# Kernel tuning notes

Hardware: AMD Instinct MI355X
Metric: run time of the kernel (lower is better)

Reference implementation:

```python
import jax, jax.numpy as jnp
import numpy as np

B, S, E, H = 8, 1024, 768, 12
D = E // H  # per-head dim


def setup_inputs() -> dict:
    key = jax.random.key(0)
    ks = jax.random.split(key, 9)
    glorot = lambda k: jax.random.normal(k, (E, E), jnp.float32) * np.sqrt(2.0 / (E + E))
    return {
        "inputs": jax.random.normal(ks[0], (B, S, E), jnp.float32),
        "Wq": glorot(ks[1]), "bq": jnp.zeros((E,), jnp.float32),
        "Wk": glorot(ks[2]), "bk": jnp.zeros((E,), jnp.float32),
        "Wv": glorot(ks[3]), "bv": jnp.zeros((E,), jnp.float32),
        "Wo": glorot(ks[4]), "bo": jnp.zeros((E,), jnp.float32),
    }


def reference(inputs, Wq, bq, Wk, bk, Wv, bv, Wo, bo):
    b, s, e = inputs.shape
    # QKV projections then split heads: [B,S,E] -> [B,H,S,D]
    def heads(x):
        return x.reshape(b, s, H, D).transpose(0, 2, 1, 3)
    q = heads(inputs @ Wq + bq)
    k = heads(inputs @ Wk + bk)
    v = heads(inputs @ Wv + bv)
    scale = 1.0 / jnp.sqrt(jnp.asarray(D, inputs.dtype))
    scores = jnp.einsum("bhqd,bhkd->bhqk", q, k) * scale
    weights = jax.nn.softmax(scores, axis=-1)  # attn_drop rate 0 -> identity
    attn = jnp.einsum("bhqk,bhkd->bhqd", weights, v)
    concat = attn.transpose(0, 2, 1, 3).reshape(b, s, e)
    out = concat @ Wo + bo  # proj_drop rate 0 -> identity
    return out
```

## Files before the change

kernel.cpp:

```cpp
#include <hip/hip_runtime.h>
#include <math.h>

#define BB 8
#define SS 1024
#define EE 768
#define HH 12
#define DD 64
#define MM (BB*SS)

typedef __attribute__((ext_vector_type(8))) short short8;
typedef __attribute__((ext_vector_type(4))) short short4v;
typedef __attribute__((ext_vector_type(4))) float f32x4;

static __device__ __forceinline__ short f2bf(float x) {
    unsigned u = __float_as_uint(x);
    u += 0x7fffu + ((u >> 16) & 1u);
    return (short)(u >> 16);
}
static __device__ __forceinline__ short f2bf_fast(float x) {
    return (short)((__float_as_uint(x) + 0x8000u) >> 16);
}

static __device__ __forceinline__ void gload_lds16(const void* g, void* l) {
    __builtin_amdgcn_global_load_lds((__attribute__((address_space(1))) void*)g,
                                     (__attribute__((address_space(3))) void*)l,
                                     16, 0, 0);
}

__global__ __launch_bounds__(256)
void cast_x(const float* __restrict__ src, short* __restrict__ dst) {
    const long i = ((long)blockIdx.x * 256 + threadIdx.x) * 4;
    float4 v = *(const float4*)&src[i];
    short4v o;
    o.x = f2bf(v.x); o.y = f2bf(v.y); o.z = f2bf(v.z); o.w = f2bf(v.w);
    *(short4v*)&dst[i] = o;
}

__global__ __launch_bounds__(256)
void wcast_t(const float* __restrict__ W0, const float* __restrict__ W1,
             const float* __restrict__ W2, const float* __restrict__ W3,
             short* __restrict__ Wt) {
    __shared__ short T[64][72];
    const int z = blockIdx.z;
    const float* sp = (z == 0) ? W0 : (z == 1) ? W1 : (z == 2) ? W2 : W3;
    short* dp = Wt + (long)z * EE * EE;
    const int i0 = blockIdx.y * 64;
    const int j0 = blockIdx.x * 64;
    const int tid = threadIdx.x;
#pragma unroll
    for (int rep = 0; rep < 4; ++rep) {
        const int r = (tid >> 4) + rep * 16;
        const int c = (tid & 15) * 4;
        float4 v = *(const float4*)&sp[(long)(i0 + r) * EE + j0 + c];
        T[c + 0][r] = f2bf(v.x);
        T[c + 1][r] = f2bf(v.y);
        T[c + 2][r] = f2bf(v.z);
        T[c + 3][r] = f2bf(v.w);
    }
    __syncthreads();
#pragma unroll
    for (int rep = 0; rep < 4; ++rep) {
        const int rr = (tid >> 4) + rep * 16;
        const int cc = (tid & 15) * 4;
        short4v o;
        o.x = T[rr][cc + 0]; o.y = T[rr][cc + 1];
        o.z = T[rr][cc + 2]; o.w = T[rr][cc + 3];
        *(short4v*)&dp[(long)(j0 + rr) * EE + i0 + cc] = o;
    }
}

#define GEMM_CORE(Abase, Bbase, row0, col0)                                     \
    f32x4 acc[4][4];                                                            \
    _Pragma("unroll") for (int i = 0; i < 4; ++i)                               \
        _Pragma("unroll") for (int j = 0; j < 4; ++j)                           \
            acc[i][j] = (f32x4){0.f, 0.f, 0.f, 0.f};                            \
    const int rm = (w & 1) * 64, cn = (w >> 1) * 64;                            \
    for (int k0 = 0; k0 < EE; k0 += 64) {                                       \
        __syncthreads();                                                        \
        _Pragma("unroll") for (int i = 0; i < 4; ++i) {                         \
            const int chunk = w * 256 + i * 64 + lane;                          \
            const int r = chunk >> 3;                                           \
            const int cs = (((chunk & 7) ^ (r & 7)) << 3);                      \
            short* ldsA = Al + (w * 256 + i * 64) * 8;                          \
            short* ldsB = Bl + (w * 256 + i * 64) * 8;                          \
            gload_lds16(&Abase[(long)(row0 + r) * EE + k0 + cs], ldsA);         \
            gload_lds16(&Bbase[(long)(col0 + r) * EE + k0 + cs], ldsB);         \
        }                                                                       \
        __syncthreads();                                                        \
        _Pragma("unroll") for (int ks = 0; ks < 2; ++ks) {                      \
            short8 af[4], bf[4];                                                \
            _Pragma("unroll") for (int t = 0; t < 4; ++t)                       \
                af[t] = *(const short8*)&Al[(rm + t * 16 + m) * 64 +            \
                                            (((ks * 4 + quad) ^ (m & 7)) << 3)]; \
            _Pragma("unroll") for (int t = 0; t < 4; ++t)                       \
                bf[t] = *(const short8*)&Bl[(cn + t * 16 + m) * 64 +            \
                                            (((ks * 4 + quad) ^ (m & 7)) << 3)]; \
            _Pragma("unroll") for (int mt = 0; mt < 4; ++mt)                    \
                _Pragma("unroll") for (int nt = 0; nt < 4; ++nt)                \
                    acc[mt][nt] = __builtin_amdgcn_mfma_f32_16x16x32_bf16(      \
                        af[mt], bf[nt], acc[mt][nt], 0, 0, 0);                  \
        }                                                                       \
    }

#define TSTRIDE 134

#define QSCALE 0.1803368801111204f

__global__ __launch_bounds__(256)
void gemm_qkv(const short* __restrict__ Xb, const short* __restrict__ Wt,
              const float* __restrict__ bq, const float* __restrict__ bk,
              const float* __restrict__ bv,
              short* __restrict__ Qb, short* __restrict__ Kb,
              short* __restrict__ Vb) {
    __shared__ short SMEM[128 * TSTRIDE];
    short* const Al = SMEM;
    short* const Bl = SMEM + 128 * 64;
    const int tid = threadIdx.x, w = tid >> 6, lane = tid & 63;
    const int m = lane & 15, quad = lane >> 4;
    const int wsel = blockIdx.x / 6;
    const int colt = blockIdx.x % 6;
    const int row0 = blockIdx.y * 128;
    const int col0 = colt * 128;
    const short* Wsel = Wt + (long)wsel * EE * EE;
    const float* bias = (wsel == 0) ? bq : (wsel == 1) ? bk : bv;

    GEMM_CORE(Xb, Wsel, row0, col0)

    __syncthreads();
    const int b = row0 >> 10, s0 = row0 & 1023;

    if (wsel < 2) {
        const float scale = (wsel == 0) ? QSCALE : 1.0f;
        short* QK = (wsel == 0) ? Qb : Kb;
#pragma unroll
        for (int nt = 0; nt < 4; ++nt) {
            const float bvv = bias[col0 + cn + nt * 16 + m];
#pragma unroll
            for (int mt = 0; mt < 4; ++mt)
#pragma unroll
                for (int r = 0; r < 4; ++r)
                    SMEM[(rm + mt * 16 + quad * 4 + r) * TSTRIDE + cn + nt * 16 + m] =
                        f2bf((acc[mt][nt][r] + bvv) * scale);
        }
        __syncthreads();
#pragma unroll
        for (int rep = 0; rep < 8; ++rep) {
            const int chunk = tid + rep * 256;
            const int row = chunk >> 4;
            const int cc = (chunk & 15) * 8;
            const int colg = col0 + cc;
            const int h = colg >> 6, d = colg & 63;
            short8 v = *(const short8*)&SMEM[row * TSTRIDE + cc];
            *(short8*)&QK[((long)(b * HH + h) * SS + s0 + row) * DD + d] = v;
        }
    } else {
#pragma unroll
        for (int nt = 0; nt < 4; ++nt) {
            const float bvv = bias[col0 + cn + nt * 16 + m];
#pragma unroll
            for (int mt = 0; mt < 4; ++mt) {
                const int rowb = rm + mt * 16 + quad * 4;
                short4v o;
                o.x = f2bf(acc[mt][nt][0] + bvv);
                o.y = f2bf(acc[mt][nt][1] + bvv);
                o.z = f2bf(acc[mt][nt][2] + bvv);
                o.w = f2bf(acc[mt][nt][3] + bvv);
                *(short4v*)&SMEM[(cn + nt * 16 + m) * TSTRIDE + rowb] = o;
            }
        }
        __syncthreads();
#pragma unroll
        for (int rep = 0; rep < 8; ++rep) {
            const int chunk = tid + rep * 256;
            const int col = chunk >> 4;
            const int sc8 = (chunk & 15) * 8;
            const int colg = col0 + col;
            const int h = colg >> 6, d = colg & 63;
            short8 v = *(const short8*)&SMEM[col * TSTRIDE + sc8];
            *(short8*)&Vb[((long)(b * HH + h) * DD + d) * SS + s0 + sc8] = v;
        }
    }
}

__global__ __launch_bounds__(256)
void gemm_proj(const short* __restrict__ Cb, const short* __restrict__ WoT,
               const float* __restrict__ bo, float* __restrict__ out) {
    __shared__ short Al[128 * 64];
    __shared__ short Bl[128 * 64];
    const int tid = threadIdx.x, w = tid >> 6, lane = tid & 63;
    const int m = lane & 15, quad = lane >> 4;
    const int row0 = blockIdx.y * 128;
    const int col0 = blockIdx.x * 128;

    GEMM_CORE(Cb, WoT, row0, col0)

#pragma unroll
    for (int nt = 0; nt < 4; ++nt) {
        const int colg = col0 + cn + nt * 16 + m;
        const float bvv = bo[colg];
#pragma unroll
        for (int mt = 0; mt < 4; ++mt)
#pragma unroll
            for (int r = 0; r < 4; ++r) {
                const int srow = row0 + rm + mt * 16 + quad * 4 + r;
                out[(long)srow * EE + colg] = acc[mt][nt][r] + bvv;
            }
    }
}

__global__ __launch_bounds__(256)
void attn_mfma(const short* __restrict__ Q,
               const short* __restrict__ K,
               const short* __restrict__ Vt,
               short* __restrict__ out) {
    __shared__ short Kl[64 * 72];
    __shared__ short Vl[64 * 72];
    __shared__ short Pl[4 * 32 * 72];

    const int tid  = threadIdx.x;
    const int w    = tid >> 6;
    const int l    = tid & 63;
    const int m    = l & 15;
    const int quad = l >> 4;
    const int h = blockIdx.y, b = blockIdx.z;
    const int q0 = blockIdx.x * 128;
    const long bh = (long)(b * HH + h);

    const short* Qg = Q  + bh * SS * DD;
    const short* Kg = K  + bh * SS * DD;
    const short* Vg = Vt + bh * DD * SS;

    short8 aq[2][2];
#pragma unroll
    for (int g = 0; g < 2; ++g) {
        const int row = q0 + w * 32 + g * 16 + m;
        aq[g][0] = *(const short8*)(Qg + (long)row * DD + quad * 8);
        aq[g][1] = *(const short8*)(Qg + (long)row * DD + 32 + quad * 8);
    }

    short8 ones;
#pragma unroll
    for (int i = 0; i < 8; ++i) ones[i] = (short)0x3F80;

    f32x4 O[2][4], lacc[2];
#pragma unroll
    for (int g = 0; g < 2; ++g) {
        lacc[g] = (f32x4){0.f, 0.f, 0.f, 0.f};
#pragma unroll
        for (int dt = 0; dt < 4; ++dt) O[g][dt] = (f32x4){0.f, 0.f, 0.f, 0.f};
    }

    for (int kt = 0; kt < 16; ++kt) {
        const int k0 = kt * 64;
        __syncthreads();
#pragma unroll
        for (int rep = 0; rep < 2; ++rep) {
            const int seg = tid + rep * 256;
            const int r = seg >> 3, s = seg & 7;
            *(short8*)(Kl + r * 72 + s * 8) =
                *(const short8*)(Kg + (long)(k0 + r) * DD + s * 8);
            *(short8*)(Vl + r * 72 + s * 8) =
                *(const short8*)(Vg + (long)r * SS + k0 + s * 8);
        }
        __syncthreads();

        f32x4 sc[2][4];
#pragma unroll
        for (int nt = 0; nt < 4; ++nt) {
            const short* kb = Kl + (nt * 16 + m) * 72 + quad * 8;
            short8 b0 = *(const short8*)kb;
            short8 b1 = *(const short8*)(kb + 32);
#pragma unroll
            for (int g = 0; g < 2; ++g) {
                f32x4 a = (f32x4){0.f, 0.f, 0.f, 0.f};
                a = __builtin_amdgcn_mfma_f32_16x16x32_bf16(aq[g][0], b0, a, 0, 0, 0);
                a = __builtin_amdgcn_mfma_f32_16x16x32_bf16(aq[g][1], b1, a, 0, 0, 0);
                sc[g][nt] = a;
            }
        }

#pragma unroll
        for (int g = 0; g < 2; ++g)
#pragma unroll
            for (int nt = 0; nt < 4; ++nt)
#pragma unroll
                for (int r = 0; r < 4; ++r)
                    sc[g][nt][r] = __builtin_amdgcn_exp2f(sc[g][nt][r]);

        short* Pw = Pl + w * 32 * 72;
#pragma unroll
        for (int g = 0; g < 2; ++g)
#pragma unroll
            for (int nt = 0; nt < 4; ++nt)
#pragma unroll
                for (int r = 0; r < 4; ++r)
                    Pw[(g * 16 + quad * 4 + r) * 72 + nt * 16 + m] =
                        f2bf_fast(sc[g][nt][r]);

        short8 ap[2][2];
#pragma unroll
        for (int g = 0; g < 2; ++g) {
            ap[g][0] = *(const short8*)(Pw + (g * 16 + m) * 72 + quad * 8);
            ap[g][1] = *(const short8*)(Pw + (g * 16 + m) * 72 + 32 + quad * 8);
        }

#pragma unroll
        for (int g = 0; g < 2; ++g) {
            lacc[g] = __builtin_amdgcn_mfma_f32_16x16x32_bf16(ap[g][0], ones, lacc[g], 0, 0, 0);
            lacc[g] = __builtin_amdgcn_mfma_f32_16x16x32_bf16(ap[g][1], ones, lacc[g], 0, 0, 0);
        }
#pragma unroll
        for (int dt = 0; dt < 4; ++dt) {
            const short* vb = Vl + (dt * 16 + m) * 72 + quad * 8;
            short8 b0 = *(const short8*)vb;
            short8 b1 = *(const short8*)(vb + 32);
#pragma unroll
            for (int g = 0; g < 2; ++g) {
                O[g][dt] = __builtin_amdgcn_mfma_f32_16x16x32_bf16(ap[g][0], b0, O[g][dt], 0, 0, 0);
                O[g][dt] = __builtin_amdgcn_mfma_f32_16x16x32_bf16(ap[g][1], b1, O[g][dt], 0, 0, 0);
            }
        }
    }

#pragma unroll
    for (int g = 0; g < 2; ++g)
#pragma unroll
        for (int r = 0; r < 4; ++r) {
            const float inv = 1.0f / lacc[g][r];
            const int qo = q0 + w * 32 + g * 16 + quad * 4 + r;
            short* orow = out + ((long)(b * SS + qo)) * EE + h * DD;
#pragma unroll
            for (int dt = 0; dt < 4; ++dt)
                orow[dt * 16 + m] = f2bf(O[g][dt][r] * inv);
        }
}

extern "C" void kernel_launch(void* const* d_in, const int* in_sizes, int n_in,
                              void* d_out, int out_size, void* d_ws, size_t ws_size,
                              hipStream_t stream) {
    const float* X  = (const float*)d_in[0];
    const float* Wq = (const float*)d_in[1];
    const float* bq = (const float*)d_in[2];
    const float* Wk = (const float*)d_in[3];
    const float* bk = (const float*)d_in[4];
    const float* Wv = (const float*)d_in[5];
    const float* bv = (const float*)d_in[6];
    const float* Wo = (const float*)d_in[7];
    const float* bo = (const float*)d_in[8];

    const long SEG = (long)BB * HH * SS * DD;
    const long WSEG = (long)EE * EE;
    short* Xb = (short*)d_ws;
    short* Wt = Xb + SEG;
    short* Qb = Wt + 4 * WSEG;
    short* Kb = Qb + SEG;
    short* Vb = Kb + SEG;
    short* Cb = Vb + SEG;

    cast_x<<<dim3(MM * EE / 4 / 256), 256, 0, stream>>>(X, Xb);
    wcast_t<<<dim3(12, 12, 4), 256, 0, stream>>>(Wq, Wk, Wv, Wo, Wt);

    gemm_qkv<<<dim3(18, 64), 256, 0, stream>>>(Xb, Wt, bq, bk, bv, Qb, Kb, Vb);

    attn_mfma<<<dim3(SS / 128, HH, BB), 256, 0, stream>>>(Qb, Kb, Vb, Cb);

    gemm_proj<<<dim3(6, 64), 256, 0, stream>>>(Cb, Wt + 3 * WSEG, bo,
                                               (float*)d_out);
}
```

Before: 216.1 us.

## Merge cast kernels, swap MFMA operands for vectorized epilogues, pad LDS strides

Folds the X cast and the weight transpose-cast into one prep launch, which saves a kernel launch. The Q/K and output-projection GEMMs swap the MFMA operands so each lane holds 4 consecutive columns. That lets the bias be read as a float4 and results be written as short4 or float4 instead of scalar stores. LDS strides for the QKV transpose buffer and the attention P buffer change to reduce bank conflicts. The risk is that the altered layouts introduce new conflicts and that the merged prep kernel branches on block index.

```diff
diff --git a/kernel.cpp b/kernel.cpp
--- a/kernel.cpp
+++ b/kernel.cpp
@@ -27,26 +27,30 @@
                                      16, 0, 0);
 }
 
+#define XB (MM * EE / 4 / 256)
+
 __global__ __launch_bounds__(256)
-void cast_x(const float* __restrict__ src, short* __restrict__ dst) {
-    const long i = ((long)blockIdx.x * 256 + threadIdx.x) * 4;
-    float4 v = *(const float4*)&src[i];
-    short4v o;
-    o.x = f2bf(v.x); o.y = f2bf(v.y); o.z = f2bf(v.z); o.w = f2bf(v.w);
-    *(short4v*)&dst[i] = o;
-}
-
-__global__ __launch_bounds__(256)
-void wcast_t(const float* __restrict__ W0, const float* __restrict__ W1,
-             const float* __restrict__ W2, const float* __restrict__ W3,
-             short* __restrict__ Wt) {
+void prep(const float* __restrict__ X,
+          const float* __restrict__ W0, const float* __restrict__ W1,
+          const float* __restrict__ W2, const float* __restrict__ W3,
+          short* __restrict__ Xb, short* __restrict__ Wt) {
     __shared__ short T[64][72];
-    const int z = blockIdx.z;
+    const int tid = threadIdx.x;
+    if ((int)blockIdx.x < XB) {
+        const long i = ((long)blockIdx.x * 256 + tid) * 4;
+        float4 v = *(const float4*)&X[i];
+        short4v o;
+        o.x = f2bf(v.x); o.y = f2bf(v.y); o.z = f2bf(v.z); o.w = f2bf(v.w);
+        *(short4v*)&Xb[i] = o;
+        return;
+    }
+    const int idx = blockIdx.x - XB;
+    const int z = idx / 144;
+    const int rem = idx % 144;
+    const int i0 = (rem / 12) * 64;
+    const int j0 = (rem % 12) * 64;
     const float* sp = (z == 0) ? W0 : (z == 1) ? W1 : (z == 2) ? W2 : W3;
     short* dp = Wt + (long)z * EE * EE;
-    const int i0 = blockIdx.y * 64;
-    const int j0 = blockIdx.x * 64;
-    const int tid = threadIdx.x;
 #pragma unroll
     for (int rep = 0; rep < 4; ++rep) {
         const int r = (tid >> 4) + rep * 16;
@@ -69,7 +73,7 @@
     }
 }
 
-#define GEMM_CORE(Abase, Bbase, row0, col0)                                     \
+#define GEMM_CORE(Abase, Bbase, row0, col0, SWAP)                               \
     f32x4 acc[4][4];                                                            \
     _Pragma("unroll") for (int i = 0; i < 4; ++i)                               \
         _Pragma("unroll") for (int j = 0; j < 4; ++j)                           \
@@ -97,12 +101,15 @@
                                             (((ks * 4 + quad) ^ (m & 7)) << 3)]; \
             _Pragma("unroll") for (int mt = 0; mt < 4; ++mt)                    \
                 _Pragma("unroll") for (int nt = 0; nt < 4; ++nt)                \
-                    acc[mt][nt] = __builtin_amdgcn_mfma_f32_16x16x32_bf16(      \
-                        af[mt], bf[nt], acc[mt][nt], 0, 0, 0);                  \
+                    acc[mt][nt] = (SWAP)                                        \
+                        ? __builtin_amdgcn_mfma_f32_16x16x32_bf16(              \
+                              bf[nt], af[mt], acc[mt][nt], 0, 0, 0)             \
+                        : __builtin_amdgcn_mfma_f32_16x16x32_bf16(              \
+                              af[mt], bf[nt], acc[mt][nt], 0, 0, 0);            \
         }                                                                       \
     }
 
-#define TSTRIDE 134
+#define TS 140
 
 #define QSCALE 0.1803368801111204f
 
@@ -112,7 +119,7 @@
               const float* __restrict__ bv,
               short* __restrict__ Qb, short* __restrict__ Kb,
               short* __restrict__ Vb) {
-    __shared__ short SMEM[128 * TSTRIDE];
+    __shared__ short SMEM[128 * TS];
     short* const Al = SMEM;
     short* const Bl = SMEM + 128 * 64;
     const int tid = threadIdx.x, w = tid >> 6, lane = tid & 63;
@@ -122,25 +129,26 @@
     const int row0 = blockIdx.y * 128;
     const int col0 = colt * 128;
     const short* Wsel = Wt + (long)wsel * EE * EE;
-    const float* bias = (wsel == 0) ? bq : (wsel == 1) ? bk : bv;
-
-    GEMM_CORE(Xb, Wsel, row0, col0)
-
-    __syncthreads();
     const int b = row0 >> 10, s0 = row0 & 1023;
 
     if (wsel < 2) {
+        const float* bias = (wsel == 0) ? bq : bk;
         const float scale = (wsel == 0) ? QSCALE : 1.0f;
         short* QK = (wsel == 0) ? Qb : Kb;
+        GEMM_CORE(Xb, Wsel, row0, col0, 1)
+        __syncthreads();
 #pragma unroll
         for (int nt = 0; nt < 4; ++nt) {
-            const float bvv = bias[col0 + cn + nt * 16 + m];
-#pragma unroll
-            for (int mt = 0; mt < 4; ++mt)
-#pragma unroll
-                for (int r = 0; r < 4; ++r)
-                    SMEM[(rm + mt * 16 + quad * 4 + r) * TSTRIDE + cn + nt * 16 + m] =
-                        f2bf((acc[mt][nt][r] + bvv) * scale);
+            float4 b4 = *(const float4*)&bias[col0 + cn + nt * 16 + quad * 4];
+#pragma unroll
+            for (int mt = 0; mt < 4; ++mt) {
+                short4v o;
+                o.x = f2bf((acc[mt][nt][0] + b4.x) * scale);
+                o.y = f2bf((acc[mt][nt][1] + b4.y) * scale);
+                o.z = f2bf((acc[mt][nt][2] + b4.z) * scale);
+                o.w = f2bf((acc[mt][nt][3] + b4.w) * scale);
+                *(short4v*)&SMEM[(rm + mt * 16 + m) * TS + cn + nt * 16 + quad * 4] = o;
+            }
         }
         __syncthreads();
 #pragma unroll
@@ -150,13 +158,15 @@
             const int cc = (chunk & 15) * 8;
             const int colg = col0 + cc;
             const int h = colg >> 6, d = colg & 63;
-            short8 v = *(const short8*)&SMEM[row * TSTRIDE + cc];
+            short8 v = *(const short8*)&SMEM[row * TS + cc];
             *(short8*)&QK[((long)(b * HH + h) * SS + s0 + row) * DD + d] = v;
         }
     } else {
+        GEMM_CORE(Xb, Wsel, row0, col0, 0)
+        __syncthreads();
 #pragma unroll
         for (int nt = 0; nt < 4; ++nt) {
-            const float bvv = bias[col0 + cn + nt * 16 + m];
+            const float bvv = bv[col0 + cn + nt * 16 + m];
 #pragma unroll
             for (int mt = 0; mt < 4; ++mt) {
                 const int rowb = rm + mt * 16 + quad * 4;
@@ -165,7 +175,7 @@
                 o.y = f2bf(acc[mt][nt][1] + bvv);
                 o.z = f2bf(acc[mt][nt][2] + bvv);
                 o.w = f2bf(acc[mt][nt][3] + bvv);
-                *(short4v*)&SMEM[(cn + nt * 16 + m) * TSTRIDE + rowb] = o;
+                *(short4v*)&SMEM[(cn + nt * 16 + m) * TS + rowb] = o;
             }
         }
         __syncthreads();
@@ -176,7 +186,7 @@
             const int sc8 = (chunk & 15) * 8;
             const int colg = col0 + col;
             const int h = colg >> 6, d = colg & 63;
-            short8 v = *(const short8*)&SMEM[col * TSTRIDE + sc8];
+            short8 v = *(const short8*)&SMEM[col * TS + sc8];
             *(short8*)&Vb[((long)(b * HH + h) * DD + d) * SS + s0 + sc8] = v;
         }
     }
@@ -192,21 +202,26 @@
     const int row0 = blockIdx.y * 128;
     const int col0 = blockIdx.x * 128;
 
-    GEMM_CORE(Cb, WoT, row0, col0)
+    GEMM_CORE(Cb, WoT, row0, col0, 1)
 
 #pragma unroll
     for (int nt = 0; nt < 4; ++nt) {
-        const int colg = col0 + cn + nt * 16 + m;
-        const float bvv = bo[colg];
-#pragma unroll
-        for (int mt = 0; mt < 4; ++mt)
-#pragma unroll
-            for (int r = 0; r < 4; ++r) {
-                const int srow = row0 + rm + mt * 16 + quad * 4 + r;
-                out[(long)srow * EE + colg] = acc[mt][nt][r] + bvv;
-            }
-    }
-}
+        const int colg = col0 + cn + nt * 16 + quad * 4;
+        float4 b4 = *(const float4*)&bo[colg];
+#pragma unroll
+        for (int mt = 0; mt < 4; ++mt) {
+            const int srow = row0 + rm + mt * 16 + m;
+            float4 v;
+            v.x = acc[mt][nt][0] + b4.x;
+            v.y = acc[mt][nt][1] + b4.y;
+            v.z = acc[mt][nt][2] + b4.z;
+            v.w = acc[mt][nt][3] + b4.w;
+            *(float4*)&out[(long)srow * EE + colg] = v;
+        }
+    }
+}
+
+#define PTS 76
 
 __global__ __launch_bounds__(256)
 void attn_mfma(const short* __restrict__ Q,
@@ -215,7 +230,7 @@
                short* __restrict__ out) {
     __shared__ short Kl[64 * 72];
     __shared__ short Vl[64 * 72];
-    __shared__ short Pl[4 * 32 * 72];
+    __shared__ short Pl[4 * 32 * PTS];
 
     const int tid  = threadIdx.x;
     const int w    = tid >> 6;
@@ -287,21 +302,21 @@
                 for (int r = 0; r < 4; ++r)
                     sc[g][nt][r] = __builtin_amdgcn_exp2f(sc[g][nt][r]);
 
-        short* Pw = Pl + w * 32 * 72;
+        short* Pw = Pl + w * 32 * PTS;
 #pragma unroll
         for (int g = 0; g < 2; ++g)
 #pragma unroll
             for (int nt = 0; nt < 4; ++nt)
 #pragma unroll
                 for (int r = 0; r < 4; ++r)
-                    Pw[(g * 16 + quad * 4 + r) * 72 + nt * 16 + m] =
+                    Pw[(g * 16 + quad * 4 + r) * PTS + nt * 16 + m] =
                         f2bf_fast(sc[g][nt][r]);
 
         short8 ap[2][2];
 #pragma unroll
         for (int g = 0; g < 2; ++g) {
-            ap[g][0] = *(const short8*)(Pw + (g * 16 + m) * 72 + quad * 8);
-            ap[g][1] = *(const short8*)(Pw + (g * 16 + m) * 72 + 32 + quad * 8);
+            ap[g][0] = *(const short8*)(Pw + (g * 16 + m) * PTS + quad * 8);
+            ap[g][1] = *(const short8*)(Pw + (g * 16 + m) * PTS + 32 + quad * 8);
         }
 
 #pragma unroll
@@ -357,8 +372,7 @@
     short* Vb = Kb + SEG;
     short* Cb = Vb + SEG;
 
-    cast_x<<<dim3(MM * EE / 4 / 256), 256, 0, stream>>>(X, Xb);
-    wcast_t<<<dim3(12, 12, 4), 256, 0, stream>>>(Wq, Wk, Wv, Wo, Wt);
+    prep<<<dim3(XB + 576), 256, 0, stream>>>(X, Wq, Wk, Wv, Wo, Xb, Wt);
 
     gemm_qkv<<<dim3(18, 64), 256, 0, stream>>>(Xb, Wt, bq, bk, bv, Qb, Kb, Vb);
 
```

Result: slower. 232.0 us (+7.4%).
